# Kernel tuning notes

Hardware: AMD Instinct MI355X
Metric: run time of the kernel (lower is better)

Reference implementation:

```python
import jax, jax.numpy as jnp
import numpy as np

D_MODEL, D_FF, H, B, S = 1024, 4096, 16, 4, 2048
D_K = D_MODEL // H
EPS = 1e-5
NEG = -1e9


def _custom_ln(x, alpha, bias):
    # torch: mean, std (unbiased, N-1), alpha*(x-mean)/(std+eps)+bias; alpha/bias scalars
    mean = jnp.mean(x, axis=-1, keepdims=True)
    n = x.shape[-1]
    var = jnp.sum((x - mean) ** 2, axis=-1, keepdims=True) / (n - 1)
    std = jnp.sqrt(var)
    return alpha * (x - mean) / (std + EPS) + bias


def setup_inputs() -> dict:
    key = jax.random.key(0)
    ks = jax.random.split(key, 12)
    sc_d = 1.0 / np.sqrt(D_MODEL)
    sc_f = 1.0 / np.sqrt(D_FF)
    inp = {
        "x": jax.random.normal(ks[0], (B, S, D_MODEL), jnp.float32),
        "src_mask": jnp.ones((B, 1, 1, S), jnp.int32),
        "wq": jax.random.normal(ks[1], (D_MODEL, D_MODEL), jnp.float32) * sc_d,
        "bq": jnp.zeros((D_MODEL,), jnp.float32),
        "wk": jax.random.normal(ks[2], (D_MODEL, D_MODEL), jnp.float32) * sc_d,
        "bk": jnp.zeros((D_MODEL,), jnp.float32),
        "wv": jax.random.normal(ks[3], (D_MODEL, D_MODEL), jnp.float32) * sc_d,
        "bv": jnp.zeros((D_MODEL,), jnp.float32),
        "wo": jax.random.normal(ks[4], (D_MODEL, D_MODEL), jnp.float32) * sc_d,
        "bo": jnp.zeros((D_MODEL,), jnp.float32),
        "w1": jax.random.normal(ks[5], (D_MODEL, D_FF), jnp.float32) * sc_d,
        "b1": jnp.zeros((D_FF,), jnp.float32),
        "w2": jax.random.normal(ks[6], (D_FF, D_MODEL), jnp.float32) * sc_f,
        "b2": jnp.zeros((D_MODEL,), jnp.float32),
        "ln1_a": jnp.ones((1,), jnp.float32),
        "ln1_b": jnp.zeros((1,), jnp.float32),
        "ln2_a": jnp.ones((1,), jnp.float32),
        "ln2_b": jnp.zeros((1,), jnp.float32),
    }
    return inp


def _attention(xn, src_mask, wq, bq, wk, bk, wv, bv, wo, bo):
    q = (xn @ wq + bq).reshape(B, S, H, D_K).transpose(0, 2, 1, 3)  # [B,H,S,Dk]
    k = (xn @ wk + bk).reshape(B, S, H, D_K).transpose(0, 2, 1, 3)
    v = (xn @ wv + bv).reshape(B, S, H, D_K).transpose(0, 2, 1, 3)
    scores = jnp.einsum("bhqd,bhkd->bhqk", q, k) / np.sqrt(D_K)
    scores = jnp.where(src_mask == 0, NEG, scores)
    attn = jax.nn.softmax(scores, axis=-1)
    ctx = jnp.einsum("bhqk,bhkd->bhqd", attn, v)
    ctx = ctx.transpose(0, 2, 1, 3).reshape(B, S, D_MODEL)
    return ctx @ wo + bo


def reference(x, src_mask, wq, bq, wk, bk, wv, bv, wo, bo,
              w1, b1, w2, b2, ln1_a, ln1_b, ln2_a, ln2_b):
    # pre-LN attention residual (dropout=0 -> identity)
    xn = _custom_ln(x, ln1_a, ln1_b)
    x = x + _attention(xn, src_mask, wq, bq, wk, bk, wv, bv, wo, bo)
    # pre-LN FFN residual
    xn = _custom_ln(x, ln2_a, ln2_b)
    ff = jax.nn.relu(xn @ w1 + b1) @ w2 + b2
    return x + ff
```

## Files before the change

kernel.cpp:

```cpp
#include <hip/hip_runtime.h>

typedef unsigned short u16;
typedef __bf16 bf16x8 __attribute__((ext_vector_type(8)));
typedef float f32x4 __attribute__((ext_vector_type(4)));

__device__ __forceinline__ u16 f2bf(float f) {
  unsigned u = __builtin_bit_cast(unsigned, f);
  unsigned lsb = (u >> 16) & 1u;
  u += 0x7fffu + lsb;
  return (u16)(u >> 16);
}

__device__ __forceinline__ unsigned cvt_pk_bf16(float lo, float hi) {
  unsigned r;
  asm("v_cvt_pk_bf16_f32 %0, %1, %2" : "=v"(r) : "v"(lo), "v"(hi));
  return r;
}

__device__ __forceinline__ void gld_lds16(const u16* g, u16* l) {
  __builtin_amdgcn_global_load_lds(
      (__attribute__((address_space(1))) void*)g,
      (__attribute__((address_space(3))) void*)l, 16, 0, 0);
}

__global__ __launch_bounds__(256) void ln_kernel(
    const float* __restrict__ x, u16* __restrict__ out,
    const float* __restrict__ alpha_p, const float* __restrict__ beta_p) {
  const int row = blockIdx.x;
  const int t = threadIdx.x;
  const float4 v = reinterpret_cast<const float4*>(x + (size_t)row * 1024)[t];
  float s = v.x + v.y + v.z + v.w;
  float sq = v.x * v.x + v.y * v.y + v.z * v.z + v.w * v.w;
#pragma unroll
  for (int off = 32; off > 0; off >>= 1) {
    s += __shfl_down(s, off);
    sq += __shfl_down(sq, off);
  }
  __shared__ float red[8];
  const int w = t >> 6;
  if ((t & 63) == 0) { red[w] = s; red[4 + w] = sq; }
  __syncthreads();
  const float ts = red[0] + red[1] + red[2] + red[3];
  const float tq = red[4] + red[5] + red[6] + red[7];
  const float mean = ts * (1.0f / 1024.0f);
  float var = (tq - ts * mean) * (1.0f / 1023.0f);
  var = fmaxf(var, 0.0f);
  const float rden = 1.0f / (sqrtf(var) + 1e-5f);
  const float a = alpha_p[0], bb = beta_p[0];
  uint2 ov;
  ov.x = cvt_pk_bf16(a * (v.x - mean) * rden + bb, a * (v.y - mean) * rden + bb);
  ov.y = cvt_pk_bf16(a * (v.z - mean) * rden + bb, a * (v.w - mean) * rden + bb);
  reinterpret_cast<uint2*>(out + (size_t)row * 1024)[t] = ov;
}

__global__ __launch_bounds__(256) void wcvt_t(
    const float* __restrict__ w, u16* __restrict__ wt, int K, int N, float scale) {
  __shared__ float tile[32][33];
  const int n0 = blockIdx.x * 32, k0 = blockIdx.y * 32;
  const int tx = threadIdx.x, ty = threadIdx.y;
#pragma unroll
  for (int i = 0; i < 4; ++i)
    tile[ty + i * 8][tx] = w[(size_t)(k0 + ty + i * 8) * N + n0 + tx];
  __syncthreads();
#pragma unroll
  for (int i = 0; i < 4; ++i)
    wt[(size_t)(n0 + ty + i * 8) * K + k0 + tx] = f2bf(tile[tx][ty + i * 8] * scale);
}

__global__ __launch_bounds__(256) void pack_bias(
    const float* __restrict__ a, const float* __restrict__ b,
    const float* __restrict__ c, float* __restrict__ o, float qscale) {
  const int i = blockIdx.x * 256 + threadIdx.x;
  o[i] = (i < 1024) ? a[i] * qscale : ((i < 2048) ? b[i - 1024] : c[i - 2048]);
}

__global__ __launch_bounds__(256) void mk_mbias(
    const int* __restrict__ mask, float* __restrict__ mb, int* __restrict__ flags) {
  const int b = blockIdx.x, t = threadIdx.x;
  __shared__ int bad;
  if (t == 0) bad = 0;
  __syncthreads();
  int loc = 0;
#pragma unroll
  for (int i = 0; i < 8; ++i) {
    const int idx = b * 2048 + t * 8 + i;
    const int mv = mask[idx];
    mb[idx] = mv ? 0.f : -1.4427e9f;
    loc |= (mv == 0);
  }
  if (loc) atomicOr(&bad, 1);
  __syncthreads();
  if (t == 0) flags[b] = !bad;
}

template <int EPI, int BM>
__global__ __launch_bounds__(512, (BM == 256) ? 2 : 4) void gemm8(
    const u16* __restrict__ A, const u16* __restrict__ Bt,
    const float* __restrict__ bias, const float* __restrict__ res,
    void* __restrict__ Cout, u16* __restrict__ vt, int M, int N, int K) {
  constexpr int BN = 256;
  constexpr int NA = BM / 128;
  constexpr int NB = 2;
  constexpr int VMC = NA + NB;
  constexpr int MF = BM / 32;
  extern __shared__ u16 smem[];
  u16* Asb = smem;
  u16* Bsb = smem + 3 * BM * 32;

  const int tid = threadIdx.x;
  const int l = tid & 63;
  const int w = tid >> 6;
  const int wr = w >> 2, wc = w & 3;
  const int gx = gridDim.x;
  int id = blockIdx.y * gx + blockIdx.x;
  const int nwg = gx * gridDim.y;
  id = (id & 7) * (nwg >> 3) + (id >> 3);
  const int n0 = (id % gx) * BN;
  const int m0 = (id / gx) * BM;
  const int lr = l & 15, lg = l >> 4;
  const int koff = (lg ^ ((lr >> 1) & 3)) * 8;

  f32x4 acc[MF][4];
#pragma unroll
  for (int i = 0; i < MF; ++i)
#pragma unroll
    for (int j = 0; j < 4; ++j) acc[i][j] = f32x4{0.f, 0.f, 0.f, 0.f};

  const u16* aSrc[NA];
  int aOff[NA];
#pragma unroll
  for (int i = 0; i < NA; ++i) {
    const int ci = tid + i * 512;
    const int row = ci >> 2, c = ci & 3;
    const int sc = c ^ ((row >> 1) & 3);
    aSrc[i] = A + (size_t)(m0 + row) * K + sc * 8;
    aOff[i] = ci * 8;
  }
  const u16* bSrc[NB];
  int bOff[NB];
#pragma unroll
  for (int i = 0; i < NB; ++i) {
    const int ci = tid + i * 512;
    const int row = ci >> 2, c = ci & 3;
    const int sc = c ^ ((row >> 1) & 3);
    bSrc[i] = Bt + (size_t)(n0 + row) * K + sc * 8;
    bOff[i] = ci * 8;
  }

  const int NT = K >> 5;
#pragma unroll
  for (int i = 0; i < NA; ++i) gld_lds16(aSrc[i], Asb + aOff[i]);
#pragma unroll
  for (int i = 0; i < NB; ++i) gld_lds16(bSrc[i], Bsb + bOff[i]);
#pragma unroll
  for (int i = 0; i < NA; ++i) gld_lds16(aSrc[i] + 32, Asb + BM * 32 + aOff[i]);
#pragma unroll
  for (int i = 0; i < NB; ++i) gld_lds16(bSrc[i] + 32, Bsb + BN * 32 + bOff[i]);
  if constexpr (VMC == 4) asm volatile("s_waitcnt vmcnt(4)" ::: "memory");
  else asm volatile("s_waitcnt vmcnt(3)" ::: "memory");
  __builtin_amdgcn_s_barrier();

  int cur = 0;
  for (int t = 0; t < NT; ++t) {
    const int nx2 = (cur + 2 >= 3) ? cur - 1 : cur + 2;
    if (t + 2 < NT) {
      const int ko = (t + 2) * 32;
#pragma unroll
      for (int i = 0; i < NA; ++i) gld_lds16(aSrc[i] + ko, Asb + nx2 * BM * 32 + aOff[i]);
#pragma unroll
      for (int i = 0; i < NB; ++i) gld_lds16(bSrc[i] + ko, Bsb + nx2 * BN * 32 + bOff[i]);
    }
    const u16* Ab = Asb + cur * BM * 32;
    const u16* Bb = Bsb + cur * BN * 32;
    bf16x8 a[MF], b[4];
#pragma unroll
    for (int mf = 0; mf < MF; ++mf)
      a[mf] = *reinterpret_cast<const bf16x8*>(&Ab[(wr * (BM / 2) + mf * 16 + lr) * 32 + koff]);
#pragma unroll
    for (int nf = 0; nf < 4; ++nf)
      b[nf] = *reinterpret_cast<const bf16x8*>(&Bb[(wc * 64 + nf * 16 + lr) * 32 + koff]);
    __builtin_amdgcn_s_setprio(1);
#pragma unroll
    for (int mf = 0; mf < MF; ++mf)
#pragma unroll
      for (int nf = 0; nf < 4; ++nf)
        acc[mf][nf] = __builtin_amdgcn_mfma_f32_16x16x32_bf16(a[mf], b[nf], acc[mf][nf], 0, 0, 0);
    __builtin_amdgcn_s_setprio(0);
    if (t + 2 < NT) {
      if constexpr (VMC == 4) asm volatile("s_waitcnt vmcnt(4)" ::: "memory");
      else asm volatile("s_waitcnt vmcnt(3)" ::: "memory");
    } else {
      asm volatile("s_waitcnt vmcnt(0)" ::: "memory");
    }
    __builtin_amdgcn_s_barrier();
    cur = (cur + 1 >= 3) ? 0 : cur + 1;
  }

  if (EPI == 3 && n0 >= 2048) {
#pragma unroll
    for (int mf = 0; mf < MF; ++mf) {
#pragma unroll
      for (int nf = 0; nf < 4; ++nf) {
        const int col = n0 + wc * 64 + nf * 16 + lr;
        const float bv = bias[col];
        const int row0 = m0 + wr * (BM / 2) + mf * 16 + lg * 4;
        const int bb = row0 >> 11, s0 = row0 & 2047;
        const int d = col - 2048;
        uint2 pv;
        pv.x = cvt_pk_bf16(acc[mf][nf][0] + bv, acc[mf][nf][1] + bv);
        pv.y = cvt_pk_bf16(acc[mf][nf][2] + bv, acc[mf][nf][3] + bv);
        *reinterpret_cast<uint2*>(vt + ((size_t)bb * 1024 + d) * 2048 + s0) = pv;
      }
    }
    return;
  }

#pragma unroll
  for (int mf = 0; mf < MF; ++mf) {
#pragma unroll
    for (int nf = 0; nf < 4; ++nf) {
      const int col = n0 + wc * 64 + nf * 16 + lr;
      const float bv = bias[col];
#pragma unroll
      for (int j = 0; j < 4; ++j) {
        const int row = m0 + wr * (BM / 2) + mf * 16 + lg * 4 + j;
        const size_t idx = (size_t)row * N + col;
        const float vv = acc[mf][nf][j] + bv;
        if (EPI == 1)
          ((float*)Cout)[idx] = vv + res[idx];
        else if (EPI == 2)
          ((u16*)Cout)[idx] = f2bf(fmaxf(vv, 0.f));
        else
          ((u16*)Cout)[idx] = f2bf(vv);
      }
    }
  }
}

__global__ __launch_bounds__(512, 4) void attn_fwd9(
    const u16* __restrict__ qkv, const u16* __restrict__ vt,
    const float* __restrict__ mbias, const int* __restrict__ flags,
    u16* __restrict__ ctx) {
  __shared__ u16 Ks[2][64 * 64];
  __shared__ u16 Vs[2][64 * 64];
  const int tid = threadIdx.x;
  const int l = tid & 63;
  const int w = tid >> 6;
  const int p = blockIdx.y * 8 + blockIdx.x;
  const int idx = p >> 3;
  const int bh = (p & 7) * 8 + (idx >> 3);
  const int qx = idx & 7;
  const int b = bh >> 4, h = bh & 15;
  const int r0 = qx * 256 + w * 32;
  const int lr = l & 15, lg = l >> 4;

  const u16* qb = qkv + (size_t)b * 2048 * 3072 + h * 64;
  const u16* kp = qb + 1024;
  const u16* vb = vt + ((size_t)b * 1024 + h * 64) * 2048;
  const float* mb = mbias + (size_t)b * 2048;
  const int allLive = flags[b];

  bf16x8 qf[2][2];
#pragma unroll
  for (int m = 0; m < 2; ++m)
#pragma unroll
    for (int ks = 0; ks < 2; ++ks)
      qf[m][ks] = *reinterpret_cast<const bf16x8*>(
          qb + (size_t)(r0 + m * 16 + lr) * 3072 + ks * 32 + lg * 8);

  bf16x8 ones;
#pragma unroll
  for (int e = 0; e < 8; ++e) ones[e] = (__bf16)1.0f;

  float mrun[2] = {-1e30f, -1e30f};
  f32x4 osum[2];
  f32x4 o[2][4];
#pragma unroll
  for (int m = 0; m < 2; ++m) {
    osum[m] = f32x4{0.f, 0.f, 0.f, 0.f};
#pragma unroll
    for (int d = 0; d < 4; ++d) o[m][d] = f32x4{0.f, 0.f, 0.f, 0.f};
  }

  const int srow = tid >> 3, scc = tid & 7;
  const int ssc = scc ^ (srow & 7);
  const u16* kS = kp + (size_t)srow * 3072 + ssc * 8;
  const u16* vS = vb + (size_t)srow * 2048 + ssc * 8;
  gld_lds16(kS, &Ks[0][tid * 8]);
  gld_lds16(vS, &Vs[0][tid * 8]);
  asm volatile("s_waitcnt vmcnt(0)" ::: "memory");
  __syncthreads();

  union U8 { unsigned u[4]; bf16x8 v; };

  int cur = 0;
  for (int t = 0; t < 32; ++t) {
    const int kb0 = t * 64;
    if (t + 1 < 32) {
      const int nb = kb0 + 64;
      gld_lds16(kS + (size_t)nb * 3072, &Ks[cur ^ 1][tid * 8]);
      gld_lds16(vS + nb, &Vs[cur ^ 1][tid * 8]);
    }

    f32x4 st[2][4];
    __builtin_amdgcn_s_setprio(1);
#pragma unroll
    for (int cf = 0; cf < 4; ++cf) {
      const int krow = cf * 16 + lr;
      const int ch0 = lg ^ (krow & 7);
      const int ch1 = (4 + lg) ^ (krow & 7);
      const bf16x8 kf0 = *reinterpret_cast<const bf16x8*>(&Ks[cur][krow * 64 + ch0 * 8]);
      const bf16x8 kf1 = *reinterpret_cast<const bf16x8*>(&Ks[cur][krow * 64 + ch1 * 8]);
#pragma unroll
      for (int m = 0; m < 2; ++m) {
        f32x4 acc = __builtin_amdgcn_mfma_f32_16x16x32_bf16(kf0, qf[m][0],
                                                            f32x4{0.f, 0.f, 0.f, 0.f}, 0, 0, 0);
        st[m][cf] = __builtin_amdgcn_mfma_f32_16x16x32_bf16(kf1, qf[m][1], acc, 0, 0, 0);
      }
    }
    __builtin_amdgcn_s_setprio(0);

    if (!allLive) {
#pragma unroll
      for (int cf = 0; cf < 4; ++cf) {
        const float4 m4 = *reinterpret_cast<const float4*>(mb + kb0 + cf * 16 + lg * 4);
#pragma unroll
        for (int m = 0; m < 2; ++m) {
          st[m][cf][0] += m4.x;
          st[m][cf][1] += m4.y;
          st[m][cf][2] += m4.z;
          st[m][cf][3] += m4.w;
        }
      }
    }

    bf16x8 paA[2], paB[2];
#pragma unroll
    for (int m = 0; m < 2; ++m) {
      float p0 = fmaxf(fmaxf(st[m][0][0], st[m][0][1]), st[m][0][2]);
      float p1 = fmaxf(fmaxf(st[m][0][3], st[m][1][0]), st[m][1][1]);
      float p2 = fmaxf(fmaxf(st[m][1][2], st[m][1][3]), st[m][2][0]);
      float p3 = fmaxf(fmaxf(st[m][2][1], st[m][2][2]), st[m][2][3]);
      float p4 = fmaxf(fmaxf(st[m][3][0], st[m][3][1]), st[m][3][2]);
      float pm = fmaxf(fmaxf(p0, p1), p2);
      pm = fmaxf(fmaxf(pm, p3), p4);
      pm = fmaxf(pm, st[m][3][3]);
      pm = fmaxf(pm, __shfl_xor(pm, 16));
      pm = fmaxf(pm, __shfl_xor(pm, 32));
      if (__any(pm > mrun[m] + 8.f)) {
        const float mn = fmaxf(mrun[m], pm);
        const float corr = exp2f(mrun[m] - mn);
        mrun[m] = mn;
#pragma unroll
        for (int j = 0; j < 4; ++j) osum[m][j] *= corr;
#pragma unroll
        for (int d = 0; d < 4; ++d)
#pragma unroll
          for (int j = 0; j < 4; ++j) o[m][d][j] *= corr;
      }
#pragma unroll
      for (int cf = 0; cf < 4; ++cf)
#pragma unroll
        for (int j = 0; j < 4; ++j)
          st[m][cf][j] = exp2f(st[m][cf][j] - mrun[m]);

      unsigned pk[4][2];
#pragma unroll
      for (int cf = 0; cf < 4; ++cf)
#pragma unroll
        for (int wp = 0; wp < 2; ++wp)
          pk[cf][wp] = cvt_pk_bf16(st[m][cf][2 * wp], st[m][cf][2 * wp + 1]);

      U8 a0, a1;
#pragma unroll
      for (int c = 0; c < 2; ++c) {
        const int src = lr + 16 * ((2 * lg + c) & 3);
#pragma unroll
        for (int wp = 0; wp < 2; ++wp) {
          const int v00 = __shfl((int)pk[0][wp], src);
          const int v01 = __shfl((int)pk[1][wp], src);
          const int v10 = __shfl((int)pk[2][wp], src);
          const int v11 = __shfl((int)pk[3][wp], src);
          a0.u[2 * c + wp] = (unsigned)((lg < 2) ? v00 : v01);
          a1.u[2 * c + wp] = (unsigned)((lg < 2) ? v10 : v11);
        }
      }
      paA[m] = a0.v;
      paB[m] = a1.v;
    }

    __builtin_amdgcn_s_setprio(1);
#pragma unroll
    for (int df = 0; df < 4; ++df) {
      const int vrow = df * 16 + lr;
      const int ch0 = lg ^ (vrow & 7);
      const int ch1 = (4 + lg) ^ (vrow & 7);
      const bf16x8 vf0 = *reinterpret_cast<const bf16x8*>(&Vs[cur][vrow * 64 + ch0 * 8]);
      const bf16x8 vf1 = *reinterpret_cast<const bf16x8*>(&Vs[cur][vrow * 64 + ch1 * 8]);
#pragma unroll
      for (int m = 0; m < 2; ++m) {
        o[m][df] = __builtin_amdgcn_mfma_f32_16x16x32_bf16(vf0, paA[m], o[m][df], 0, 0, 0);
        o[m][df] = __builtin_amdgcn_mfma_f32_16x16x32_bf16(vf1, paB[m], o[m][df], 0, 0, 0);
      }
    }
#pragma unroll
    for (int m = 0; m < 2; ++m) {
      osum[m] = __builtin_amdgcn_mfma_f32_16x16x32_bf16(ones, paA[m], osum[m], 0, 0, 0);
      osum[m] = __builtin_amdgcn_mfma_f32_16x16x32_bf16(ones, paB[m], osum[m], 0, 0, 0);
    }
    __builtin_amdgcn_s_setprio(0);

    asm volatile("s_waitcnt vmcnt(0)" ::: "memory");
    __syncthreads();
    cur ^= 1;
  }

#pragma unroll
  for (int m = 0; m < 2; ++m) {
    const float rdiv = 1.f / osum[m][0];
    const size_t rowbase = ((size_t)b * 2048 + r0 + m * 16 + lr) * 1024 + h * 64;
#pragma unroll
    for (int df = 0; df < 4; ++df) {
      uint2 s4;
      s4.x = cvt_pk_bf16(o[m][df][0] * rdiv, o[m][df][1] * rdiv);
      s4.y = cvt_pk_bf16(o[m][df][2] * rdiv, o[m][df][3] * rdiv);
      *reinterpret_cast<uint2*>(ctx + rowbase + df * 16 + lg * 4) = s4;
    }
  }
}

extern "C" void kernel_launch(void* const* d_in, const int* in_sizes, int n_in,
                              void* d_out, int out_size, void* d_ws, size_t ws_size,
                              hipStream_t stream) {
  const float* x = (const float*)d_in[0];
  const int* mask = (const int*)d_in[1];
  const float* wq = (const float*)d_in[2];
  const float* bq = (const float*)d_in[3];
  const float* wk = (const float*)d_in[4];
  const float* bk = (const float*)d_in[5];
  const float* wv = (const float*)d_in[6];
  const float* bv = (const float*)d_in[7];
  const float* wo = (const float*)d_in[8];
  const float* bo = (const float*)d_in[9];
  const float* w1 = (const float*)d_in[10];
  const float* b1 = (const float*)d_in[11];
  const float* w2 = (const float*)d_in[12];
  const float* b2 = (const float*)d_in[13];
  const float* ln1a = (const float*)d_in[14];
  const float* ln1b = (const float*)d_in[15];
  const float* ln2a = (const float*)d_in[16];
  const float* ln2b = (const float*)d_in[17];

  const float SCL2 = 0.125f * 1.4426950408889634f;
  const size_t LDS256 = 3 * (256 + 256) * 32 * sizeof(u16);
  const size_t LDS128 = 3 * (128 + 256) * 32 * sizeof(u16);

  hipFuncSetAttribute((const void*)&gemm8<3, 128>,
                      hipFuncAttributeMaxDynamicSharedMemorySize, (int)LDS128);
  hipFuncSetAttribute((const void*)&gemm8<2, 256>,
                      hipFuncAttributeMaxDynamicSharedMemorySize, (int)LDS256);
  hipFuncSetAttribute((const void*)&gemm8<1, 128>,
                      hipFuncAttributeMaxDynamicSharedMemorySize, (int)LDS128);

  char* ws = (char*)d_ws;
  const size_t MB = 1024ull * 1024ull;
  u16* WTQKV = (u16*)(ws + 0 * MB);
  u16* WTO = (u16*)(ws + 6 * MB);
  u16* W1T = (u16*)(ws + 8 * MB);
  u16* W2T = (u16*)(ws + 16 * MB);
  float* BQKV = (float*)(ws + 24 * MB);
  float* MBIAS = (float*)(ws + 24 * MB + 65536);
  int* FLAGS = (int*)(ws + 24 * MB + 131072);
  u16* QKV = (u16*)(ws + 25 * MB);
  u16* VT = (u16*)(ws + 73 * MB);
  u16* XN = (u16*)(ws + 89 * MB);
  u16* CTX = (u16*)(ws + 105 * MB);
  float* X2 = (float*)(ws + 25 * MB);
  u16* XN2 = (u16*)(ws + 57 * MB);
  u16* H1 = (u16*)(ws + 73 * MB);

  dim3 bt(32, 8);
  wcvt_t<<<dim3(32, 32), bt, 0, stream>>>(wq, WTQKV, 1024, 1024, SCL2);
  wcvt_t<<<dim3(32, 32), bt, 0, stream>>>(wk, WTQKV + 1024 * 1024, 1024, 1024, 1.f);
  wcvt_t<<<dim3(32, 32), bt, 0, stream>>>(wv, WTQKV + 2048 * 1024, 1024, 1024, 1.f);
  wcvt_t<<<dim3(32, 32), bt, 0, stream>>>(wo, WTO, 1024, 1024, 1.f);
  wcvt_t<<<dim3(128, 32), bt, 0, stream>>>(w1, W1T, 1024, 4096, 1.f);
  wcvt_t<<<dim3(32, 128), bt, 0, stream>>>(w2, W2T, 4096, 1024, 1.f);
  pack_bias<<<dim3(12), 256, 0, stream>>>(bq, bk, bv, BQKV, SCL2);
  mk_mbias<<<dim3(4), 256, 0, stream>>>(mask, MBIAS, FLAGS);

  ln_kernel<<<8192, 256, 0, stream>>>(x, XN, ln1a, ln1b);
  gemm8<3, 128><<<dim3(12, 64), 512, LDS128, stream>>>(XN, WTQKV, BQKV, nullptr, QKV, VT, 8192, 3072, 1024);
  attn_fwd9<<<dim3(8, 64), 512, 0, stream>>>(QKV, VT, MBIAS, FLAGS, CTX);
  gemm8<1, 128><<<dim3(4, 64), 512, LDS128, stream>>>(CTX, WTO, bo, x, X2, nullptr, 8192, 1024, 1024);
  ln_kernel<<<8192, 256, 0, stream>>>(X2, XN2, ln2a, ln2b);
  gemm8<2, 256><<<dim3(16, 32), 512, LDS256, stream>>>(XN2, W1T, b1, nullptr, H1, nullptr, 8192, 4096, 1024);
  gemm8<1, 128><<<dim3(4, 64), 512, LDS128, stream>>>(H1, W2T, b2, X2, (float*)d_out, nullptr, 8192, 1024, 4096);
}
```

Before: 443.4 us.

## Add 4-stage two-tile-per-barrier GEMM for residual outputs, use BM=128 for FFN1

Adds a new gemm9 kernel for the residual-add GEMMs (output projection and FFN2). It uses a 4-deep LDS ring, prefetches two K-tiles per iteration and computes two tiles per barrier, which halves the barrier count and deepens the prefetch. The FFN1 GEMM switches from BM=256 at occupancy 2 to BM=128 at occupancy 4 with twice the grid, and the templated BM is removed. The costs are more LDS for gemm9 and more re-reads of B tiles in FFN1.

```diff
diff --git a/kernel.cpp b/kernel.cpp
--- a/kernel.cpp
+++ b/kernel.cpp
@@ -93,16 +93,13 @@
   if (t == 0) flags[b] = !bad;
 }
 
-template <int EPI, int BM>
-__global__ __launch_bounds__(512, (BM == 256) ? 2 : 4) void gemm8(
+template <int EPI>
+__global__ __launch_bounds__(512, 4) void gemm8(
     const u16* __restrict__ A, const u16* __restrict__ Bt,
     const float* __restrict__ bias, const float* __restrict__ res,
     void* __restrict__ Cout, u16* __restrict__ vt, int M, int N, int K) {
-  constexpr int BN = 256;
-  constexpr int NA = BM / 128;
-  constexpr int NB = 2;
-  constexpr int VMC = NA + NB;
-  constexpr int MF = BM / 32;
+  constexpr int BM = 128, BN = 256;
+  constexpr int MF = 4;
   extern __shared__ u16 smem[];
   u16* Asb = smem;
   u16* Bsb = smem + 3 * BM * 32;
@@ -126,20 +123,19 @@
 #pragma unroll
     for (int j = 0; j < 4; ++j) acc[i][j] = f32x4{0.f, 0.f, 0.f, 0.f};
 
-  const u16* aSrc[NA];
-  int aOff[NA];
-#pragma unroll
-  for (int i = 0; i < NA; ++i) {
-    const int ci = tid + i * 512;
+  const u16* aSrc;
+  int aOff;
+  {
+    const int ci = tid;
     const int row = ci >> 2, c = ci & 3;
     const int sc = c ^ ((row >> 1) & 3);
-    aSrc[i] = A + (size_t)(m0 + row) * K + sc * 8;
-    aOff[i] = ci * 8;
-  }
-  const u16* bSrc[NB];
-  int bOff[NB];
-#pragma unroll
-  for (int i = 0; i < NB; ++i) {
+    aSrc = A + (size_t)(m0 + row) * K + sc * 8;
+    aOff = ci * 8;
+  }
+  const u16* bSrc[2];
+  int bOff[2];
+#pragma unroll
+  for (int i = 0; i < 2; ++i) {
     const int ci = tid + i * 512;
     const int row = ci >> 2, c = ci & 3;
     const int sc = c ^ ((row >> 1) & 3);
@@ -148,16 +144,13 @@
   }
 
   const int NT = K >> 5;
-#pragma unroll
-  for (int i = 0; i < NA; ++i) gld_lds16(aSrc[i], Asb + aOff[i]);
-#pragma unroll
-  for (int i = 0; i < NB; ++i) gld_lds16(bSrc[i], Bsb + bOff[i]);
-#pragma unroll
-  for (int i = 0; i < NA; ++i) gld_lds16(aSrc[i] + 32, Asb + BM * 32 + aOff[i]);
-#pragma unroll
-  for (int i = 0; i < NB; ++i) gld_lds16(bSrc[i] + 32, Bsb + BN * 32 + bOff[i]);
-  if constexpr (VMC == 4) asm volatile("s_waitcnt vmcnt(4)" ::: "memory");
-  else asm volatile("s_waitcnt vmcnt(3)" ::: "memory");
+  gld_lds16(aSrc, Asb + aOff);
+#pragma unroll
+  for (int i = 0; i < 2; ++i) gld_lds16(bSrc[i], Bsb + bOff[i]);
+  gld_lds16(aSrc + 32, Asb + BM * 32 + aOff);
+#pragma unroll
+  for (int i = 0; i < 2; ++i) gld_lds16(bSrc[i] + 32, Bsb + BN * 32 + bOff[i]);
+  asm volatile("s_waitcnt vmcnt(3)" ::: "memory");
   __builtin_amdgcn_s_barrier();
 
   int cur = 0;
@@ -165,10 +158,9 @@
     const int nx2 = (cur + 2 >= 3) ? cur - 1 : cur + 2;
     if (t + 2 < NT) {
       const int ko = (t + 2) * 32;
-#pragma unroll
-      for (int i = 0; i < NA; ++i) gld_lds16(aSrc[i] + ko, Asb + nx2 * BM * 32 + aOff[i]);
-#pragma unroll
-      for (int i = 0; i < NB; ++i) gld_lds16(bSrc[i] + ko, Bsb + nx2 * BN * 32 + bOff[i]);
+      gld_lds16(aSrc + ko, Asb + nx2 * BM * 32 + aOff);
+#pragma unroll
+      for (int i = 0; i < 2; ++i) gld_lds16(bSrc[i] + ko, Bsb + nx2 * BN * 32 + bOff[i]);
     }
     const u16* Ab = Asb + cur * BM * 32;
     const u16* Bb = Bsb + cur * BN * 32;
@@ -186,12 +178,8 @@
       for (int nf = 0; nf < 4; ++nf)
         acc[mf][nf] = __builtin_amdgcn_mfma_f32_16x16x32_bf16(a[mf], b[nf], acc[mf][nf], 0, 0, 0);
     __builtin_amdgcn_s_setprio(0);
-    if (t + 2 < NT) {
-      if constexpr (VMC == 4) asm volatile("s_waitcnt vmcnt(4)" ::: "memory");
-      else asm volatile("s_waitcnt vmcnt(3)" ::: "memory");
-    } else {
-      asm volatile("s_waitcnt vmcnt(0)" ::: "memory");
-    }
+    if (t + 2 < NT) asm volatile("s_waitcnt vmcnt(3)" ::: "memory");
+    else asm volatile("s_waitcnt vmcnt(0)" ::: "memory");
     __builtin_amdgcn_s_barrier();
     cur = (cur + 1 >= 3) ? 0 : cur + 1;
   }
@@ -226,12 +214,140 @@
         const int row = m0 + wr * (BM / 2) + mf * 16 + lg * 4 + j;
         const size_t idx = (size_t)row * N + col;
         const float vv = acc[mf][nf][j] + bv;
-        if (EPI == 1)
-          ((float*)Cout)[idx] = vv + res[idx];
-        else if (EPI == 2)
+        if (EPI == 2)
           ((u16*)Cout)[idx] = f2bf(fmaxf(vv, 0.f));
         else
           ((u16*)Cout)[idx] = f2bf(vv);
+      }
+    }
+  }
+}
+
+__global__ __launch_bounds__(512, 4) void gemm9(
+    const u16* __restrict__ A, const u16* __restrict__ Bt,
+    const float* __restrict__ bias, const float* __restrict__ res,
+    float* __restrict__ Cout, int M, int N, int K) {
+  constexpr int BM = 128, BN = 256;
+  constexpr int MF = 4;
+  extern __shared__ u16 smem[];
+  u16* Asb = smem;
+  u16* Bsb = smem + 4 * BM * 32;
+
+  const int tid = threadIdx.x;
+  const int l = tid & 63;
+  const int w = tid >> 6;
+  const int wr = w >> 2, wc = w & 3;
+  const int gx = gridDim.x;
+  int id = blockIdx.y * gx + blockIdx.x;
+  const int nwg = gx * gridDim.y;
+  id = (id & 7) * (nwg >> 3) + (id >> 3);
+  const int n0 = (id % gx) * BN;
+  const int m0 = (id / gx) * BM;
+  const int lr = l & 15, lg = l >> 4;
+  const int koff = (lg ^ ((lr >> 1) & 3)) * 8;
+
+  f32x4 acc[MF][4];
+#pragma unroll
+  for (int i = 0; i < MF; ++i)
+#pragma unroll
+    for (int j = 0; j < 4; ++j) acc[i][j] = f32x4{0.f, 0.f, 0.f, 0.f};
+
+  const u16* aSrc;
+  int aOff;
+  {
+    const int ci = tid;
+    const int row = ci >> 2, c = ci & 3;
+    const int sc = c ^ ((row >> 1) & 3);
+    aSrc = A + (size_t)(m0 + row) * K + sc * 8;
+    aOff = ci * 8;
+  }
+  const u16* bSrc[2];
+  int bOff[2];
+#pragma unroll
+  for (int i = 0; i < 2; ++i) {
+    const int ci = tid + i * 512;
+    const int row = ci >> 2, c = ci & 3;
+    const int sc = c ^ ((row >> 1) & 3);
+    bSrc[i] = Bt + (size_t)(n0 + row) * K + sc * 8;
+    bOff[i] = ci * 8;
+  }
+
+  const int NT = K >> 5;
+  gld_lds16(aSrc, Asb + aOff);
+#pragma unroll
+  for (int i = 0; i < 2; ++i) gld_lds16(bSrc[i], Bsb + bOff[i]);
+  gld_lds16(aSrc + 32, Asb + BM * 32 + aOff);
+#pragma unroll
+  for (int i = 0; i < 2; ++i) gld_lds16(bSrc[i] + 32, Bsb + BN * 32 + bOff[i]);
+
+  for (int t = 0; t < NT; t += 2) {
+    const int b0 = t & 3, b1 = (t + 1) & 3, b2 = (t + 2) & 3, b3 = (t + 3) & 3;
+    if (t + 2 < NT) asm volatile("s_waitcnt vmcnt(3)" ::: "memory");
+    else asm volatile("s_waitcnt vmcnt(3)" ::: "memory");
+    __builtin_amdgcn_s_barrier();
+    if (t + 2 < NT) {
+      const int ko2 = (t + 2) * 32;
+      gld_lds16(aSrc + ko2, Asb + b2 * BM * 32 + aOff);
+#pragma unroll
+      for (int i = 0; i < 2; ++i) gld_lds16(bSrc[i] + ko2, Bsb + b2 * BN * 32 + bOff[i]);
+      if (t + 3 < NT) {
+        const int ko3 = (t + 3) * 32;
+        gld_lds16(aSrc + ko3, Asb + b3 * BM * 32 + aOff);
+#pragma unroll
+        for (int i = 0; i < 2; ++i) gld_lds16(bSrc[i] + ko3, Bsb + b3 * BN * 32 + bOff[i]);
+      }
+    }
+    {
+      const u16* Ab = Asb + b0 * BM * 32;
+      const u16* Bb = Bsb + b0 * BN * 32;
+      bf16x8 a[MF], b[4];
+#pragma unroll
+      for (int mf = 0; mf < MF; ++mf)
+        a[mf] = *reinterpret_cast<const bf16x8*>(&Ab[(wr * (BM / 2) + mf * 16 + lr) * 32 + koff]);
+#pragma unroll
+      for (int nf = 0; nf < 4; ++nf)
+        b[nf] = *reinterpret_cast<const bf16x8*>(&Bb[(wc * 64 + nf * 16 + lr) * 32 + koff]);
+      __builtin_amdgcn_s_setprio(1);
+#pragma unroll
+      for (int mf = 0; mf < MF; ++mf)
+#pragma unroll
+        for (int nf = 0; nf < 4; ++nf)
+          acc[mf][nf] = __builtin_amdgcn_mfma_f32_16x16x32_bf16(a[mf], b[nf], acc[mf][nf], 0, 0, 0);
+      __builtin_amdgcn_s_setprio(0);
+    }
+    if (t + 2 < NT) asm volatile("s_waitcnt vmcnt(6)" ::: "memory");
+    else asm volatile("s_waitcnt vmcnt(0)" ::: "memory");
+    {
+      const u16* Ab = Asb + b1 * BM * 32;
+      const u16* Bb = Bsb + b1 * BN * 32;
+      bf16x8 a[MF], b[4];
+#pragma unroll
+      for (int mf = 0; mf < MF; ++mf)
+        a[mf] = *reinterpret_cast<const bf16x8*>(&Ab[(wr * (BM / 2) + mf * 16 + lr) * 32 + koff]);
+#pragma unroll
+      for (int nf = 0; nf < 4; ++nf)
+        b[nf] = *reinterpret_cast<const bf16x8*>(&Bb[(wc * 64 + nf * 16 + lr) * 32 + koff]);
+      __builtin_amdgcn_s_setprio(1);
+#pragma unroll
+      for (int mf = 0; mf < MF; ++mf)
+#pragma unroll
+        for (int nf = 0; nf < 4; ++nf)
+          acc[mf][nf] = __builtin_amdgcn_mfma_f32_16x16x32_bf16(a[mf], b[nf], acc[mf][nf], 0, 0, 0);
+      __builtin_amdgcn_s_setprio(0);
+    }
+  }
+
+#pragma unroll
+  for (int mf = 0; mf < MF; ++mf) {
+#pragma unroll
+    for (int nf = 0; nf < 4; ++nf) {
+      const int col = n0 + wc * 64 + nf * 16 + lr;
+      const float bv = bias[col];
+#pragma unroll
+      for (int j = 0; j < 4; ++j) {
+        const int row = m0 + wr * (BM / 2) + mf * 16 + lg * 4 + j;
+        const size_t idx = (size_t)row * N + col;
+        Cout[idx] = acc[mf][nf][j] + bv + res[idx];
       }
     }
   }
@@ -452,15 +568,15 @@
   const float* ln2b = (const float*)d_in[17];
 
   const float SCL2 = 0.125f * 1.4426950408889634f;
-  const size_t LDS256 = 3 * (256 + 256) * 32 * sizeof(u16);
-  const size_t LDS128 = 3 * (128 + 256) * 32 * sizeof(u16);
-
-  hipFuncSetAttribute((const void*)&gemm8<3, 128>,
-                      hipFuncAttributeMaxDynamicSharedMemorySize, (int)LDS128);
-  hipFuncSetAttribute((const void*)&gemm8<2, 256>,
-                      hipFuncAttributeMaxDynamicSharedMemorySize, (int)LDS256);
-  hipFuncSetAttribute((const void*)&gemm8<1, 128>,
-                      hipFuncAttributeMaxDynamicSharedMemorySize, (int)LDS128);
+  const size_t LDS128_3 = 3 * (128 + 256) * 32 * sizeof(u16);
+  const size_t LDS128_4 = 4 * (128 + 256) * 32 * sizeof(u16);
+
+  hipFuncSetAttribute((const void*)&gemm8<3>,
+                      hipFuncAttributeMaxDynamicSharedMemorySize, (int)LDS128_3);
+  hipFuncSetAttribute((const void*)&gemm8<2>,
+                      hipFuncAttributeMaxDynamicSharedMemorySize, (int)LDS128_3);
+  hipFuncSetAttribute((const void*)&gemm9,
+                      hipFuncAttributeMaxDynamicSharedMemorySize, (int)LDS128_4);
 
   char* ws = (char*)d_ws;
   const size_t MB = 1024ull * 1024ull;
@@ -490,10 +606,10 @@
   mk_mbias<<<dim3(4), 256, 0, stream>>>(mask, MBIAS, FLAGS);
 
   ln_kernel<<<8192, 256, 0, stream>>>(x, XN, ln1a, ln1b);
-  gemm8<3, 128><<<dim3(12, 64), 512, LDS128, stream>>>(XN, WTQKV, BQKV, nullptr, QKV, VT, 8192, 3072, 1024);
+  gemm8<3><<<dim3(12, 64), 512, LDS128_3, stream>>>(XN, WTQKV, BQKV, nullptr, QKV, VT, 8192, 3072, 1024);
   attn_fwd9<<<dim3(8, 64), 512, 0, stream>>>(QKV, VT, MBIAS, FLAGS, CTX);
-  gemm8<1, 128><<<dim3(4, 64), 512, LDS128, stream>>>(CTX, WTO, bo, x, X2, nullptr, 8192, 1024, 1024);
+  gemm9<<<dim3(4, 64), 512, LDS128_4, stream>>>(CTX, WTO, bo, x, X2, 8192, 1024, 1024);
   ln_kernel<<<8192, 256, 0, stream>>>(X2, XN2, ln2a, ln2b);
-  gemm8<2, 256><<<dim3(16, 32), 512, LDS256, stream>>>(XN2, W1T, b1, nullptr, H1, nullptr, 8192, 4096, 1024);
-  gemm8<1, 128><<<dim3(4, 64), 512, LDS128, stream>>>(H1, W2T, b2, X2, (float*)d_out, nullptr, 8192, 1024, 4096);
-}
+  gemm8<2><<<dim3(16, 64), 512, LDS128_3, stream>>>(XN2, W1T, b1, nullptr, H1, nullptr, 8192, 4096, 1024);
+  gemm9<<<dim3(4, 64), 512, LDS128_4, stream>>>(H1, W2T, b2, X2, (float*)d_out, 8192, 1024, 4096);
+}
```

Result: no change. 451.4 us (+1.8%).
